# Kernel tuning notes

Measured on AMD Instinct MI355X. Metric: run time of the kernel, lower is better.

The kernel has to match this reference:

```python
import jax, jax.numpy as jnp
import numpy as np

S, C1, C2, N = 4096, 2048, 2048, 1024


def setup_inputs() -> dict:
    key = jax.random.key(0)
    k1, k2, k3, k4 = jax.random.split(key, 4)
    # child log-likelihoods (samples, child_nodes); modest scale so exp() stays finite,
    # matching the (numerically naive) torch forward which exps without max-subtraction.
    ll1 = jax.random.normal(k1, (S, C1), dtype=jnp.float32)
    ll2 = jax.random.normal(k2, (S, C2), dtype=jnp.float32)
    # log edge weights, one tensor per child layer: (nodes, child_nodes)
    w1 = jax.random.normal(k3, (N, C1), dtype=jnp.float32)
    w2 = jax.random.normal(k4, (N, C2), dtype=jnp.float32)
    return {"ll1": ll1, "ll2": ll2, "w1": w1, "w2": w2}


def reference(ll1, ll2, w1, w2):
    # Per child layer: sum_c exp(ll[s,c] + w[n,c]) == exp(ll) @ exp(w).T  -> (S, N)
    # (same math as unsqueeze/repeat/exp/sum in the torch code, without the (S,C,N) blowup)
    result = jnp.exp(ll1) @ jnp.exp(w1).T + jnp.exp(ll2) @ jnp.exp(w2).T  # (S, N)
    # per-node log normalization constant over concatenated weights
    log_z = jax.nn.logsumexp(jnp.concatenate([w1, w2], axis=1), axis=1)  # (N,)
    return jnp.log(result) - log_z[None, :]
```

## Files before the change

kernel.cpp:

```cpp
#include <hip/hip_runtime.h>

#define S_DIM 4096
#define C_DIM 2048
#define N_DIM 1024
#define K_DIM 4096

#define BM 128
#define BN 128
#define BK 32
#define NT (K_DIM / BK)
#define TILE_BYTES 16384
#define NBUF 8

typedef __attribute__((ext_vector_type(8))) short bf16x8;
typedef __attribute__((ext_vector_type(4))) float f32x4;

__device__ static inline unsigned short f2bf(float f) {
    unsigned int u = __float_as_uint(f);
    u += 0x7FFFu + ((u >> 16) & 1u);
    return (unsigned short)(u >> 16);
}

__global__ void exp_ll_kernel(const float* __restrict__ ll1,
                              const float* __restrict__ ll2,
                              unsigned short* __restrict__ A) {
    const int total4 = S_DIM * C_DIM / 4;
    int stride = gridDim.x * blockDim.x;
    for (int i = blockIdx.x * blockDim.x + threadIdx.x; i < total4; i += stride) {
        int e = i << 2;
        int r = e >> 11;
        int c = e & 2047;
        size_t dst = ((size_t)r << 12) + c;
        float4 v = *reinterpret_cast<const float4*>(ll1 + e);
        ushort4 o;
        o.x = f2bf(__expf(v.x)); o.y = f2bf(__expf(v.y));
        o.z = f2bf(__expf(v.z)); o.w = f2bf(__expf(v.w));
        *reinterpret_cast<ushort4*>(A + dst) = o;
        float4 u = *reinterpret_cast<const float4*>(ll2 + e);
        ushort4 p;
        p.x = f2bf(__expf(u.x)); p.y = f2bf(__expf(u.y));
        p.z = f2bf(__expf(u.z)); p.w = f2bf(__expf(u.w));
        *reinterpret_cast<ushort4*>(A + dst + C_DIM) = p;
    }
}

__global__ void w_kernel(const float* __restrict__ w1,
                         const float* __restrict__ w2,
                         unsigned short* __restrict__ B,
                         float* __restrict__ lz) {
    const int n = blockIdx.x;
    const int tid = threadIdx.x;
    const int lane = tid & 63, wv = tid >> 6;
    const float* r1 = w1 + ((size_t)n << 11);
    const float* r2 = w2 + ((size_t)n << 11);
    float4 v0 = *reinterpret_cast<const float4*>(r1 + tid * 8);
    float4 v1 = *reinterpret_cast<const float4*>(r1 + tid * 8 + 4);
    float4 u0 = *reinterpret_cast<const float4*>(r2 + tid * 8);
    float4 u1 = *reinterpret_cast<const float4*>(r2 + tid * 8 + 4);

    float mx = fmaxf(fmaxf(fmaxf(v0.x, v0.y), fmaxf(v0.z, v0.w)),
                     fmaxf(fmaxf(v1.x, v1.y), fmaxf(v1.z, v1.w)));
    mx = fmaxf(mx, fmaxf(fmaxf(fmaxf(u0.x, u0.y), fmaxf(u0.z, u0.w)),
                          fmaxf(fmaxf(u1.x, u1.y), fmaxf(u1.z, u1.w))));
    #pragma unroll
    for (int off = 32; off > 0; off >>= 1) mx = fmaxf(mx, __shfl_xor(mx, off));
    __shared__ float red[4];
    if (lane == 0) red[wv] = mx;
    __syncthreads();
    mx = fmaxf(fmaxf(red[0], red[1]), fmaxf(red[2], red[3]));

    float s = __expf(v0.x - mx) + __expf(v0.y - mx) + __expf(v0.z - mx) + __expf(v0.w - mx)
            + __expf(v1.x - mx) + __expf(v1.y - mx) + __expf(v1.z - mx) + __expf(v1.w - mx)
            + __expf(u0.x - mx) + __expf(u0.y - mx) + __expf(u0.z - mx) + __expf(u0.w - mx)
            + __expf(u1.x - mx) + __expf(u1.y - mx) + __expf(u1.z - mx) + __expf(u1.w - mx);
    #pragma unroll
    for (int off = 32; off > 0; off >>= 1) s += __shfl_xor(s, off);
    __shared__ float red2[4];
    if (lane == 0) red2[wv] = s;
    __syncthreads();
    if (tid == 0)
        lz[n] = mx + __logf(red2[0] + red2[1] + red2[2] + red2[3]);

    unsigned short* brow = B + ((size_t)n << 12);
    ushort4 o;
    o.x = f2bf(__expf(v0.x)); o.y = f2bf(__expf(v0.y));
    o.z = f2bf(__expf(v0.z)); o.w = f2bf(__expf(v0.w));
    *reinterpret_cast<ushort4*>(brow + tid * 8) = o;
    o.x = f2bf(__expf(v1.x)); o.y = f2bf(__expf(v1.y));
    o.z = f2bf(__expf(v1.z)); o.w = f2bf(__expf(v1.w));
    *reinterpret_cast<ushort4*>(brow + tid * 8 + 4) = o;
    o.x = f2bf(__expf(u0.x)); o.y = f2bf(__expf(u0.y));
    o.z = f2bf(__expf(u0.z)); o.w = f2bf(__expf(u0.w));
    *reinterpret_cast<ushort4*>(brow + C_DIM + tid * 8) = o;
    o.x = f2bf(__expf(u1.x)); o.y = f2bf(__expf(u1.y));
    o.z = f2bf(__expf(u1.z)); o.w = f2bf(__expf(u1.w));
    *reinterpret_cast<ushort4*>(brow + C_DIM + tid * 8 + 4) = o;
}

typedef const unsigned int __attribute__((address_space(1)))* gas_ptr;
typedef unsigned int __attribute__((address_space(3)))* las_ptr;

__global__ __launch_bounds__(256, 1) void gemm_log_kernel(
        const unsigned short* __restrict__ A,
        const unsigned short* __restrict__ B,
        const float* __restrict__ lz,
        float* __restrict__ out) {
    __shared__ __align__(16) char lds[NBUF * TILE_BYTES];
    const int tid  = threadIdx.x;
    const int l    = tid & 63;
    const int w    = tid >> 6;
    const int bn = blockIdx.x & 7;
    const int bm = blockIdx.x >> 3;
    const int wr = w >> 1, wc = w & 1;
    const int lcol = l & 15, lk = l >> 4;

    const int kg = (l & 3) ^ ((l >> 3) & 3);
    const unsigned short* src[4];
    int dst[4];
    #pragma unroll
    for (int i = 0; i < 4; ++i) {
        const int ri  = w * 4 + i;
        const int row = ri * 16 + (l >> 2);
        src[i] = (ri < 8)
            ? A + (size_t)(bm * BM + row) * K_DIM + kg * 8
            : B + (size_t)(bn * BN + row - 128) * K_DIM + kg * 8;
        dst[i] = row * 64 + (l & 3) * 16;
    }

    const int swz = (lk ^ ((lcol >> 1) & 3)) << 4;
    int aoff[4], boff[4];
    #pragma unroll
    for (int m = 0; m < 4; ++m) aoff[m] = (wr * 64 + m * 16 + lcol) * 64 + swz;
    #pragma unroll
    for (int n = 0; n < 4; ++n) boff[n] = 8192 + (wc * 64 + n * 16 + lcol) * 64 + swz;

    f32x4 acc[4][4] = {};

#define GLOAD(p, o) __builtin_amdgcn_global_load_lds((gas_ptr)(const void*)(p), \
        (las_ptr)(void*)(lds + (o)), 16, 0, 0)
#define STAGE(T, BUFB) { const int _ko = (T) * BK; const int _bo = (BUFB) * TILE_BYTES; \
        GLOAD(src[0] + _ko, _bo + dst[0]); GLOAD(src[1] + _ko, _bo + dst[1]);           \
        GLOAD(src[2] + _ko, _bo + dst[2]); GLOAD(src[3] + _ko, _bo + dst[3]); }
#define BODY(T, BUF, SBUF, WAITN, DOSTAGE) {                                            \
        asm volatile("s_waitcnt vmcnt(" #WAITN ")" ::: "memory");                       \
        __builtin_amdgcn_s_barrier();                                                   \
        if (DOSTAGE) STAGE((T) + 6, SBUF);                                              \
        const char* base = lds + (BUF) * TILE_BYTES;                                    \
        bf16x8 a[4], b[4];                                                              \
        _Pragma("unroll") for (int m = 0; m < 4; ++m)                                   \
            a[m] = *reinterpret_cast<const bf16x8*>(base + aoff[m]);                    \
        _Pragma("unroll") for (int n = 0; n < 4; ++n)                                   \
            b[n] = *reinterpret_cast<const bf16x8*>(base + boff[n]);                    \
        _Pragma("unroll") for (int m = 0; m < 4; ++m)                                   \
            _Pragma("unroll") for (int n = 0; n < 4; ++n)                               \
                acc[m][n] = __builtin_amdgcn_mfma_f32_16x16x32_bf16(a[m], b[n],         \
                                                                   acc[m][n], 0, 0, 0); }

    STAGE(0, 0); STAGE(1, 1); STAGE(2, 2);
    STAGE(3, 3); STAGE(4, 4); STAGE(5, 5);
    for (int t8 = 0; t8 < NT - 8; t8 += 8) {
        BODY(t8 + 0, 0, 6, 20, 1); BODY(t8 + 1, 1, 7, 20, 1);
        BODY(t8 + 2, 2, 0, 20, 1); BODY(t8 + 3, 3, 1, 20, 1);
        BODY(t8 + 4, 4, 2, 20, 1); BODY(t8 + 5, 5, 3, 20, 1);
        BODY(t8 + 6, 6, 4, 20, 1); BODY(t8 + 7, 7, 5, 20, 1);
    }
    BODY(NT - 8, 0, 6, 20, 1);
    BODY(NT - 7, 1, 7, 20, 1);
    BODY(NT - 6, 2, 0, 20, 0);
    BODY(NT - 5, 3, 0, 16, 0);
    BODY(NT - 4, 4, 0, 12, 0);
    BODY(NT - 3, 5, 0,  8, 0);
    BODY(NT - 2, 6, 0,  4, 0);
    BODY(NT - 1, 7, 0,  0, 0);
#undef BODY
#undef STAGE
#undef GLOAD

    const int col_base = bn * BN + wc * 64;
    float lzv[4];
    #pragma unroll
    for (int n = 0; n < 4; ++n) lzv[n] = lz[col_base + n * 16 + lcol];
    #pragma unroll
    for (int m = 0; m < 4; ++m) {
        const int row0 = bm * BM + wr * 64 + m * 16 + lk * 4;
        #pragma unroll
        for (int n = 0; n < 4; ++n) {
            const int col = col_base + n * 16 + lcol;
            #pragma unroll
            for (int j = 0; j < 4; ++j)
                out[(size_t)(row0 + j) * N_DIM + col] = __logf(acc[m][n][j]) - lzv[n];
        }
    }
}

__global__ void naive_kernel(const float* __restrict__ ll1, const float* __restrict__ ll2,
                             const float* __restrict__ w1, const float* __restrict__ w2,
                             float* __restrict__ out) {
    int idx = blockIdx.x * blockDim.x + threadIdx.x;
    if (idx >= S_DIM * N_DIM) return;
    int s = idx >> 10, n = idx & (N_DIM - 1);
    const float* a1 = ll1 + (size_t)s * C_DIM;
    const float* a2 = ll2 + (size_t)s * C_DIM;
    const float* b1 = w1 + (size_t)n * C_DIM;
    const float* b2 = w2 + (size_t)n * C_DIM;
    float mx = -3.0e38f;
    for (int c = 0; c < C_DIM; ++c) mx = fmaxf(mx, b1[c]);
    for (int c = 0; c < C_DIM; ++c) mx = fmaxf(mx, b2[c]);
    float zs = 0.f, acc = 0.f;
    for (int c = 0; c < C_DIM; ++c) { zs += __expf(b1[c] - mx); acc += __expf(a1[c] + b1[c]); }
    for (int c = 0; c < C_DIM; ++c) { zs += __expf(b2[c] - mx); acc += __expf(a2[c] + b2[c]); }
    out[idx] = __logf(acc) - (mx + __logf(zs));
}

extern "C" void kernel_launch(void* const* d_in, const int* in_sizes, int n_in,
                              void* d_out, int out_size, void* d_ws, size_t ws_size,
                              hipStream_t stream) {
    const float* ll1 = (const float*)d_in[0];
    const float* ll2 = (const float*)d_in[1];
    const float* w1  = (const float*)d_in[2];
    const float* w2  = (const float*)d_in[3];
    float* out = (float*)d_out;

    const size_t a_elems = (size_t)S_DIM * K_DIM;
    const size_t b_elems = (size_t)N_DIM * K_DIM;
    const size_t need = (a_elems + b_elems) * sizeof(unsigned short) + N_DIM * sizeof(float);
    if (ws_size < need) {
        naive_kernel<<<(S_DIM * N_DIM + 255) / 256, 256, 0, stream>>>(ll1, ll2, w1, w2, out);
        return;
    }
    unsigned short* Aws = (unsigned short*)d_ws;
    unsigned short* Bws = Aws + a_elems;
    float* lzws = (float*)(Bws + b_elems);

    exp_ll_kernel<<<2048, 256, 0, stream>>>(ll1, ll2, Aws);
    w_kernel<<<N_DIM, 256, 0, stream>>>(w1, w2, Bws, lzws);
    gemm_log_kernel<<<(S_DIM / BM) * (N_DIM / BN), 256, 0, stream>>>(Aws, Bws, lzws, out);
}
```

Baseline: 70.85 us.

## Double-buffer LDS fragment reads in registers and deepen global prefetch to eight stages

```diff
diff --git a/kernel.cpp b/kernel.cpp
--- a/kernel.cpp
+++ b/kernel.cpp
@@ -135,44 +135,57 @@
     for (int n = 0; n < 4; ++n) boff[n] = 8192 + (wc * 64 + n * 16 + lcol) * 64 + swz;
 
     f32x4 acc[4][4] = {};
+    bf16x8 a0[4], b0[4], a1[4], b1[4];
 
 #define GLOAD(p, o) __builtin_amdgcn_global_load_lds((gas_ptr)(const void*)(p), \
         (las_ptr)(void*)(lds + (o)), 16, 0, 0)
-#define STAGE(T, BUFB) { const int _ko = (T) * BK; const int _bo = (BUFB) * TILE_BYTES; \
+#define STAGE(T, BUFI) { const int _ko = (T) * BK; const int _bo = (BUFI) * TILE_BYTES; \
         GLOAD(src[0] + _ko, _bo + dst[0]); GLOAD(src[1] + _ko, _bo + dst[1]);           \
         GLOAD(src[2] + _ko, _bo + dst[2]); GLOAD(src[3] + _ko, _bo + dst[3]); }
-#define BODY(T, BUF, SBUF, WAITN, DOSTAGE) {                                            \
+#define READF(RBUF, AR, BR) { const char* _rb = lds + (RBUF) * TILE_BYTES;              \
+        _Pragma("unroll") for (int m = 0; m < 4; ++m)                                   \
+            AR[m] = *reinterpret_cast<const bf16x8*>(_rb + aoff[m]);                    \
+        _Pragma("unroll") for (int n = 0; n < 4; ++n)                                   \
+            BR[n] = *reinterpret_cast<const bf16x8*>(_rb + boff[n]); }
+#define MFMAS(AMM, BMM)                                                                 \
+        _Pragma("unroll") for (int m = 0; m < 4; ++m)                                   \
+            _Pragma("unroll") for (int n = 0; n < 4; ++n)                               \
+                acc[m][n] = __builtin_amdgcn_mfma_f32_16x16x32_bf16(AMM[m], BMM[n],     \
+                                                                    acc[m][n], 0, 0, 0);
+#define BODY(T, SB, RB, WAITN, DOSTAGE, AR, BR, AMM, BMM) {                             \
         asm volatile("s_waitcnt vmcnt(" #WAITN ")" ::: "memory");                       \
         __builtin_amdgcn_s_barrier();                                                   \
-        if (DOSTAGE) STAGE((T) + 6, SBUF);                                              \
-        const char* base = lds + (BUF) * TILE_BYTES;                                    \
-        bf16x8 a[4], b[4];                                                              \
-        _Pragma("unroll") for (int m = 0; m < 4; ++m)                                   \
-            a[m] = *reinterpret_cast<const bf16x8*>(base + aoff[m]);                    \
-        _Pragma("unroll") for (int n = 0; n < 4; ++n)                                   \
-            b[n] = *reinterpret_cast<const bf16x8*>(base + boff[n]);                    \
-        _Pragma("unroll") for (int m = 0; m < 4; ++m)                                   \
-            _Pragma("unroll") for (int n = 0; n < 4; ++n)                               \
-                acc[m][n] = __builtin_amdgcn_mfma_f32_16x16x32_bf16(a[m], b[n],         \
-                                                                   acc[m][n], 0, 0, 0); }
-
-    STAGE(0, 0); STAGE(1, 1); STAGE(2, 2);
-    STAGE(3, 3); STAGE(4, 4); STAGE(5, 5);
+        if (DOSTAGE) STAGE((T) + 8, SB);                                                \
+        READF(RB, AR, BR);                                                              \
+        MFMAS(AMM, BMM); }
+
+    STAGE(0, 0); STAGE(1, 1); STAGE(2, 2); STAGE(3, 3);
+    STAGE(4, 4); STAGE(5, 5); STAGE(6, 6); STAGE(7, 7);
+    asm volatile("s_waitcnt vmcnt(28)" ::: "memory");
+    __builtin_amdgcn_s_barrier();
+    READF(0, a0, b0);
+
     for (int t8 = 0; t8 < NT - 8; t8 += 8) {
-        BODY(t8 + 0, 0, 6, 20, 1); BODY(t8 + 1, 1, 7, 20, 1);
-        BODY(t8 + 2, 2, 0, 20, 1); BODY(t8 + 3, 3, 1, 20, 1);
-        BODY(t8 + 4, 4, 2, 20, 1); BODY(t8 + 5, 5, 3, 20, 1);
-        BODY(t8 + 6, 6, 4, 20, 1); BODY(t8 + 7, 7, 5, 20, 1);
-    }
-    BODY(NT - 8, 0, 6, 20, 1);
-    BODY(NT - 7, 1, 7, 20, 1);
-    BODY(NT - 6, 2, 0, 20, 0);
-    BODY(NT - 5, 3, 0, 16, 0);
-    BODY(NT - 4, 4, 0, 12, 0);
-    BODY(NT - 3, 5, 0,  8, 0);
-    BODY(NT - 2, 6, 0,  4, 0);
-    BODY(NT - 1, 7, 0,  0, 0);
+        BODY(t8 + 0, 0, 1, 24, 1, a1, b1, a0, b0);
+        BODY(t8 + 1, 1, 2, 24, 1, a0, b0, a1, b1);
+        BODY(t8 + 2, 2, 3, 24, 1, a1, b1, a0, b0);
+        BODY(t8 + 3, 3, 4, 24, 1, a0, b0, a1, b1);
+        BODY(t8 + 4, 4, 5, 24, 1, a1, b1, a0, b0);
+        BODY(t8 + 5, 5, 6, 24, 1, a0, b0, a1, b1);
+        BODY(t8 + 6, 6, 7, 24, 1, a1, b1, a0, b0);
+        BODY(t8 + 7, 7, 0, 24, 1, a0, b0, a1, b1);
+    }
+    BODY(120, 0, 1, 24, 0, a1, b1, a0, b0);
+    BODY(121, 1, 2, 20, 0, a0, b0, a1, b1);
+    BODY(122, 2, 3, 16, 0, a1, b1, a0, b0);
+    BODY(123, 3, 4, 12, 0, a0, b0, a1, b1);
+    BODY(124, 4, 5,  8, 0, a1, b1, a0, b0);
+    BODY(125, 5, 6,  4, 0, a0, b0, a1, b1);
+    BODY(126, 6, 7,  0, 0, a1, b1, a0, b0);
+    MFMAS(a1, b1);
 #undef BODY
+#undef MFMAS
+#undef READF
 #undef STAGE
 #undef GLOAD
 
```

Result: no change. 71.05 us (+0.3%).
